# Kernel tuning notes

Hardware: AMD Instinct MI355X
Metric: run time of the kernel (lower is better)

Reference implementation:

```python
import jax, jax.numpy as jnp
import numpy as np

NUM_EXPERTS = 8
TOP_K = 2
RMS_EPS = 1e-6
SCALING = NUM_EXPERTS / TOP_K


def setup_inputs() -> dict:
    key = jax.random.key(0)
    ks = jax.random.split(key, 6)
    B, S, H, I, E = 4, 2048, 2048, 1024, NUM_EXPERTS
    return {
        "hidden_states": jax.random.normal(ks[0], (B, S, H), dtype=jnp.float32),
        "norm_w": jnp.ones((H,), dtype=jnp.float32),
        "router_w": jax.random.normal(ks[1], (E, H), dtype=jnp.float32) * 0.02,
        "gate_w": jax.random.normal(ks[2], (E, I, H), dtype=jnp.float32) * 0.02,
        "up_w": jax.random.normal(ks[3], (E, I, H), dtype=jnp.float32) * 0.02,
        "down_w": jax.random.normal(ks[4], (E, H, I), dtype=jnp.float32) * 0.02,
    }


def reference(hidden_states, norm_w, router_w, gate_w, up_w, down_w):
    B, S, H = hidden_states.shape
    T = B * S
    flat = hidden_states.reshape(T, H)

    # RMSNorm on router input (fp32 math, as in torch module)
    x32 = flat.astype(jnp.float32)
    var = jnp.mean(x32 * x32, axis=-1, keepdims=True)
    router_input = norm_w * (x32 * jax.lax.rsqrt(var + RMS_EPS))

    # Router: softmax -> top-k -> renormalize
    logits = router_input @ router_w.T                     # [T, E]
    probs = jax.nn.softmax(logits, axis=-1)
    topw, topi = jax.lax.top_k(probs, TOP_K)               # [T, K]
    topw = topw / jnp.sum(topw, axis=-1, keepdims=True)

    # Expert combine: per-token weight for expert e (0 if not selected).
    # Running every token through every expert with weight-0 masking is
    # mathematically identical to the gather/scatter dispatch.
    out = jnp.zeros_like(flat)
    for e in range(NUM_EXPERTS):
        w_e = jnp.sum(jnp.where(topi == e, topw, 0.0), axis=-1)   # [T]
        g = flat @ gate_w[e].T                                    # [T, I]
        u = flat @ up_w[e].T                                      # [T, I]
        o = (jax.nn.silu(g) * u) @ down_w[e].T                    # [T, H]
        out = out + o * w_e[:, None]

    student_output = out.reshape(B, S, H) * SCALING

    # Aux load-balancing loss (training path)
    importance = jnp.sum(probs, axis=0) / T                       # [E]
    load = jnp.sum(topi[..., None] == jnp.arange(NUM_EXPERTS), axis=(0, 1)) / (T * TOP_K)
    aux_loss = jnp.sum(importance * load.astype(jnp.float32)) * NUM_EXPERTS

    return student_output, aux_loss
```

## Files before the change

### kernel.cpp

```cpp
#include <hip/hip_runtime.h>
#include <hip/hip_bf16.h>
#include <cstdint>

#define T_TOKENS 8192
#define H_DIM 2048
#define I_DIM 1024
#define N_EXPERTS 8
#define PAIRS (T_TOKENS * 2)
#define TOT_TILES 144
#define TOT_ROWS (TOT_TILES * 128)

using f32x4 = __attribute__((ext_vector_type(4))) float;
using bfv   = __attribute__((ext_vector_type(8))) short;
using u16x8 = __attribute__((ext_vector_type(8))) unsigned short;

typedef __attribute__((address_space(3))) unsigned int lds_u32;
typedef __attribute__((address_space(1))) unsigned int glb_u32;

__device__ __forceinline__ void gll16(const void* g, void* l) {
  __builtin_amdgcn_global_load_lds((const glb_u32*)g, (lds_u32*)l, 16, 0, 0);
}
#define SB0() __builtin_amdgcn_sched_barrier(0)
#define BAR() __builtin_amdgcn_s_barrier()

__device__ inline unsigned short f2bf(float f) {
  unsigned int u = __float_as_uint(f);
  u += 0x7FFFu + ((u >> 16) & 1u);
  return (unsigned short)(u >> 16);
}

__global__ __launch_bounds__(256) void moe_convert_kernel(
    const float* __restrict__ src, unsigned short* __restrict__ dst, int n8) {
  int i = blockIdx.x * 256 + threadIdx.x;
  if (i >= n8) return;
  size_t o = (size_t)i * 8;
  f32x4 a = *reinterpret_cast<const f32x4*>(src + o);
  f32x4 b = *reinterpret_cast<const f32x4*>(src + o + 4);
  u16x8 r = {f2bf(a[0]), f2bf(a[1]), f2bf(a[2]), f2bf(a[3]),
             f2bf(b[0]), f2bf(b[1]), f2bf(b[2]), f2bf(b[3])};
  *reinterpret_cast<u16x8*>(dst + o) = r;
}

__global__ __launch_bounds__(256) void moe_router_kernel(
    const float* __restrict__ X, const float* __restrict__ norm_w,
    const float* __restrict__ rw, float* __restrict__ probs,
    float* __restrict__ topw, int* __restrict__ topi,
    unsigned int* __restrict__ counts, unsigned short* __restrict__ Xb) {
  int t = blockIdx.x;
  int tid = threadIdx.x;
  const float* x = X + (size_t)t * H_DIM;
  int base = tid * 8;
  f32x4 v0 = *reinterpret_cast<const f32x4*>(x + base);
  f32x4 v1 = *reinterpret_cast<const f32x4*>(x + base + 4);
  u16x8 bx = {f2bf(v0[0]), f2bf(v0[1]), f2bf(v0[2]), f2bf(v0[3]),
              f2bf(v1[0]), f2bf(v1[1]), f2bf(v1[2]), f2bf(v1[3])};
  *reinterpret_cast<u16x8*>(Xb + (size_t)t * H_DIM + base) = bx;
  f32x4 nw0 = *reinterpret_cast<const f32x4*>(norm_w + base);
  f32x4 nw1 = *reinterpret_cast<const f32x4*>(norm_w + base + 4);
  float vals[9];
  vals[0] = v0[0]*v0[0] + v0[1]*v0[1] + v0[2]*v0[2] + v0[3]*v0[3]
          + v1[0]*v1[0] + v1[1]*v1[1] + v1[2]*v1[2] + v1[3]*v1[3];
  f32x4 a0 = v0 * nw0, a1 = v1 * nw1;
#pragma unroll
  for (int e = 0; e < 8; ++e) {
    const float* r = rw + e * H_DIM + base;
    f32x4 r0 = *reinterpret_cast<const f32x4*>(r);
    f32x4 r1 = *reinterpret_cast<const f32x4*>(r + 4);
    f32x4 d = a0 * r0 + a1 * r1;
    vals[e + 1] = d[0] + d[1] + d[2] + d[3];
  }
#pragma unroll
  for (int v = 0; v < 9; ++v) {
    float s = vals[v];
#pragma unroll
    for (int off = 32; off > 0; off >>= 1) s += __shfl_xor(s, off);
    vals[v] = s;
  }
  __shared__ float red[4][9];
  int lane = tid & 63, w = tid >> 6;
  if (lane == 0) {
#pragma unroll
    for (int v = 0; v < 9; ++v) red[w][v] = vals[v];
  }
  __syncthreads();
  if (tid == 0) {
    float tot[9];
#pragma unroll
    for (int v = 0; v < 9; ++v) tot[v] = red[0][v] + red[1][v] + red[2][v] + red[3][v];
    float rs = rsqrtf(tot[0] / (float)H_DIM + 1e-6f);
    float lg[8], mx = -1e30f;
#pragma unroll
    for (int e = 0; e < 8; ++e) { lg[e] = tot[e + 1] * rs; mx = fmaxf(mx, lg[e]); }
    float pe[8], sum = 0.f;
#pragma unroll
    for (int e = 0; e < 8; ++e) { pe[e] = expf(lg[e] - mx); sum += pe[e]; }
    float inv = 1.f / sum;
#pragma unroll
    for (int e = 0; e < 8; ++e) { pe[e] *= inv; probs[t * 8 + e] = pe[e]; }
    int b1 = 0; float p1 = pe[0];
#pragma unroll
    for (int e = 1; e < 8; ++e) if (pe[e] > p1) { p1 = pe[e]; b1 = e; }
    int b2 = -1; float p2 = -1.f;
#pragma unroll
    for (int e = 0; e < 8; ++e) if (e != b1 && pe[e] > p2) { p2 = pe[e]; b2 = e; }
    float wsum = p1 + p2;
    topw[t * 2] = p1 / wsum;
    topw[t * 2 + 1] = p2 / wsum;
    topi[t * 2] = b1;
    topi[t * 2 + 1] = b2;
    atomicAdd(&counts[b1], 1u);
    atomicAdd(&counts[8 + b2], 1u);
  }
}

__global__ __launch_bounds__(256) void moe_importance_kernel(
    const float* __restrict__ probs, float* __restrict__ impSum) {
  int e = blockIdx.x, tid = threadIdx.x;
  float s = 0.f;
  for (int t = tid; t < T_TOKENS; t += 256) s += probs[t * 8 + e];
  __shared__ float red[256];
  red[tid] = s;
  __syncthreads();
  for (int st = 128; st > 0; st >>= 1) {
    if (tid < st) red[tid] += red[tid + st];
    __syncthreads();
  }
  if (tid == 0) impSum[e] = red[0];
}

__global__ void moe_offsets_aux_kernel(const unsigned int* __restrict__ counts,
                                       const float* __restrict__ impSum,
                                       int* __restrict__ tileOff,
                                       float* __restrict__ out_aux) {
  if (threadIdx.x == 0 && blockIdx.x == 0) {
    int acc = 0;
    for (int b = 0; b < 16; ++b) {
      tileOff[b] = acc;
      acc += (int)((counts[b] + 127u) >> 7);
    }
    tileOff[16] = acc;
    float a = 0.f;
    for (int e = 0; e < 8; ++e) {
      float load = (float)(counts[e] + counts[8 + e]) / (float)PAIRS;
      a += (impSum[e] / (float)T_TOKENS) * load;
    }
    out_aux[0] = a * (float)N_EXPERTS;
  }
}

__global__ __launch_bounds__(256) void moe_assign_kernel(
    const int* __restrict__ topi, const int* __restrict__ tileOff,
    unsigned int* __restrict__ cursors, int* __restrict__ row2pair) {
  int p = blockIdx.x * 256 + threadIdx.x;
  if (p >= PAIRS) return;
  int b = topi[p] + 8 * (p & 1);
  unsigned int pos = atomicAdd(&cursors[b], 1u);
  row2pair[tileOff[b] * 128 + (int)pos] = p;
}


__global__ __launch_bounds__(256, 2) void moe_stage_a(
    const unsigned short* __restrict__ Xb,
    const unsigned short* __restrict__ Wg, const unsigned short* __restrict__ Wu,
    const int* __restrict__ row2pair, const int* __restrict__ tileOff,
    unsigned int* __restrict__ workCtr, unsigned short* __restrict__ P) {
  __shared__ __align__(16) unsigned short sAB[2][16384];
  __shared__ int sTok[128];
  __shared__ int sWork;
  const int tid = threadIdx.x;
  const int lane = tid & 63, w = tid >> 6;
  const int lrow = lane & 15, grp = lane >> 4;
  const int sub = lane >> 3;
  const int kcs = ((lane & 7) ^ sub) << 3;
  const int cx = (lane & 7) << 3;
  const int nTiles = tileOff[16];
  const int nWork = nTiles * 16;

  for (;;) {
    if (tid == 0) sWork = (int)atomicAdd(workCtr, 1u);
    __syncthreads();
    const int item = sWork;
    if (item >= nWork) break;
    const int mt = item % nTiles;
    const int nt = item / nTiles;
    int b = 0;
#pragma unroll
    for (int k = 1; k < 16; ++k) if (tileOff[k] <= mt) b = k;
    const int e = b & 7;
    const int row0 = mt * 128;
    if (tid < 128) {
      int pr = row2pair[row0 + tid];
      sTok[tid] = (pr >= 0) ? (pr >> 1) : 0;
    }
    __syncthreads();

    const size_t wbase = (size_t)e * ((size_t)I_DIM * H_DIM);
    const unsigned short* src[8];
#pragma unroll
    for (int i = 0; i < 4; ++i) {
      int row = i * 32 + 8 * w + sub;
      src[i] = Xb + (size_t)sTok[row] * H_DIM + kcs;
    }
#pragma unroll
    for (int i = 4; i < 8; ++i) {
      int brow = (i - 4) * 32 + 8 * w + sub;
      int wq = brow >> 5, r5 = brow & 31;
      int ic = nt * 64 + wq * 16 + (r5 & 15);
      const unsigned short* bp = (r5 & 16) ? Wu : Wg;
      src[i] = bp + wbase + (size_t)ic * H_DIM + kcs;
    }

    f32x4 acc[8][2] = {};

#pragma unroll
    for (int i = 0; i < 8; ++i)
      gll16(src[i], (void*)&sAB[0][(i * 256 + tid) * 8]);

    int cur = 0;
#pragma unroll 1
    for (int kk = 0; kk < 32; ++kk) {
      if (kk < 31) {
#pragma unroll
        for (int i = 0; i < 8; ++i)
          gll16(src[i] + ((kk + 1) << 6), (void*)&sAB[cur ^ 1][(i * 256 + tid) * 8]);
        SB0();
        asm volatile("s_waitcnt vmcnt(8)" ::: "memory");
      } else {
        asm volatile("s_waitcnt vmcnt(0)" ::: "memory");
      }
      SB0();
      BAR();
      SB0();
#pragma unroll
      for (int ks = 0; ks < 2; ++ks) {
        const int co = ((ks * 4 + grp) << 3) ^ cx;
        bfv af[8], bf[2];
#pragma unroll
        for (int m = 0; m < 8; ++m)
          af[m] = *reinterpret_cast<const bfv*>(&sAB[cur][(m * 16 + lrow) * 64 + co]);
#pragma unroll
        for (int n = 0; n < 2; ++n)
          bf[n] = *reinterpret_cast<const bfv*>(
              &sAB[cur][8192 + (w * 32 + n * 16 + lrow) * 64 + co]);
        __builtin_amdgcn_s_setprio(1);
#pragma unroll
        for (int m = 0; m < 8; ++m)
#pragma unroll
          for (int n = 0; n < 2; ++n)
            acc[m][n] = __builtin_amdgcn_mfma_f32_16x16x32_bf16(af[m], bf[n], acc[m][n], 0, 0, 0);
        __builtin_amdgcn_s_setprio(0);
      }
      SB0();
      BAR();
      cur ^= 1;
    }

#pragma unroll
    for (int m = 0; m < 8; ++m) {
#pragma unroll
      for (int j = 0; j < 4; ++j) {
        float g = acc[m][0][j];
        float uu = acc[m][1][j];
        float pv = (g / (1.f + expf(-g))) * uu;
        int row = row0 + m * 16 + grp * 4 + j;
        int col = nt * 64 + w * 16 + lrow;
        P[(size_t)row * I_DIM + col] = f2bf(pv);
      }
    }
  }
}

__global__ __launch_bounds__(256, 2) void moe_stage_b(
    const unsigned short* __restrict__ Pb, const unsigned short* __restrict__ Wd,
    const int* __restrict__ row2pair, const int* __restrict__ tileOff,
    const float* __restrict__ topw, unsigned int* __restrict__ workCtr,
    float* __restrict__ out, int phase) {
  __shared__ __align__(16) unsigned short sAB[2][16384];
  __shared__ int sPair[128];
  __shared__ int sWork;
  const int tid = threadIdx.x;
  const int lane = tid & 63, w = tid >> 6;
  const int lrow = lane & 15, grp = lane >> 4;
  const int sub = lane >> 3;
  const int kcs = ((lane & 7) ^ sub) << 3;
  const int cx = (lane & 7) << 3;
  const int t0 = phase ? tileOff[8] : 0;
  const int t1 = phase ? tileOff[16] : tileOff[8];
  const int nTiles = t1 - t0;
  const int nWork = nTiles * 16;

  for (;;) {
    if (tid == 0) sWork = (int)atomicAdd(workCtr, 1u);
    __syncthreads();
    const int item = sWork;
    if (item >= nWork) break;
    const int mt = t0 + item % nTiles;
    const int nt = item / nTiles;
    int b = 0;
#pragma unroll
    for (int k = 1; k < 16; ++k) if (tileOff[k] <= mt) b = k;
    const int e = b & 7;
    const int row0 = mt * 128, h0 = nt * 128;
    if (tid < 128) sPair[tid] = row2pair[row0 + tid];
    __syncthreads();

    const unsigned short* src[8];
#pragma unroll
    for (int i = 0; i < 4; ++i) {
      int row = i * 32 + 8 * w + sub;
      src[i] = Pb + (size_t)(row0 + row) * I_DIM + kcs;
    }
#pragma unroll
    for (int i = 4; i < 8; ++i) {
      int brow = (i - 4) * 32 + 8 * w + sub;
      src[i] = Wd + (size_t)e * ((size_t)H_DIM * I_DIM) + (size_t)(h0 + brow) * I_DIM + kcs;
    }

    f32x4 acc[8][2] = {};

#pragma unroll
    for (int i = 0; i < 8; ++i)
      gll16(src[i], (void*)&sAB[0][(i * 256 + tid) * 8]);

    int cur = 0;
#pragma unroll 1
    for (int kk = 0; kk < 16; ++kk) {
      if (kk < 15) {
#pragma unroll
        for (int i = 0; i < 8; ++i)
          gll16(src[i] + ((kk + 1) << 6), (void*)&sAB[cur ^ 1][(i * 256 + tid) * 8]);
        SB0();
        asm volatile("s_waitcnt vmcnt(8)" ::: "memory");
      } else {
        asm volatile("s_waitcnt vmcnt(0)" ::: "memory");
      }
      SB0();
      BAR();
      SB0();
#pragma unroll
      for (int ks = 0; ks < 2; ++ks) {
        const int co = ((ks * 4 + grp) << 3) ^ cx;
        bfv af[8], bf[2];
#pragma unroll
        for (int m = 0; m < 8; ++m)
          af[m] = *reinterpret_cast<const bfv*>(&sAB[cur][(m * 16 + lrow) * 64 + co]);
#pragma unroll
        for (int n = 0; n < 2; ++n)
          bf[n] = *reinterpret_cast<const bfv*>(
              &sAB[cur][8192 + (w * 32 + n * 16 + lrow) * 64 + co]);
        __builtin_amdgcn_s_setprio(1);
#pragma unroll
        for (int m = 0; m < 8; ++m)
#pragma unroll
          for (int n = 0; n < 2; ++n)
            acc[m][n] = __builtin_amdgcn_mfma_f32_16x16x32_bf16(af[m], bf[n], acc[m][n], 0, 0, 0);
        __builtin_amdgcn_s_setprio(0);
      }
      SB0();
      BAR();
      cur ^= 1;
    }

#pragma unroll
    for (int m = 0; m < 8; ++m) {
#pragma unroll
      for (int j = 0; j < 4; ++j) {
        int rl = m * 16 + grp * 4 + j;
        int pr = sPair[rl];
        if (pr < 0) continue;
        float wgt = topw[pr] * 4.f;
        float* orow = out + (size_t)(pr >> 1) * H_DIM + h0 + w * 32 + lrow;
        if (phase) {
#pragma unroll
          for (int n = 0; n < 2; ++n) orow[n * 16] += wgt * acc[m][n][j];
        } else {
#pragma unroll
          for (int n = 0; n < 2; ++n) orow[n * 16] = wgt * acc[m][n][j];
        }
      }
    }
  }
}

extern "C" void kernel_launch(void* const* d_in, const int* in_sizes, int n_in,
                              void* d_out, int out_size, void* d_ws, size_t ws_size,
                              hipStream_t stream) {
  const float* X = (const float*)d_in[0];
  const float* norm_w = (const float*)d_in[1];
  const float* router_w = (const float*)d_in[2];
  const float* gate_w = (const float*)d_in[3];
  const float* up_w = (const float*)d_in[4];
  const float* down_w = (const float*)d_in[5];
  float* out = (float*)d_out;

  char* ws = (char*)d_ws;
  unsigned short* P = (unsigned short*)(ws);
  float* probs = (float*)(ws + 37748736);
  float* topw = (float*)(ws + 38010880);
  int* topi = (int*)(ws + 38076416);
  int* row2pair = (int*)(ws + 38141952);
  char* ctrl = ws + 38215680;
  unsigned int* counts = (unsigned int*)(ctrl);
  unsigned int* cursors = (unsigned int*)(ctrl + 64);
  float* impSum = (float*)(ctrl + 128);
  int* tileOff = (int*)(ctrl + 192);
  unsigned int* wcA = (unsigned int*)(ctrl + 384);
  unsigned int* wcB0 = (unsigned int*)(ctrl + 388);
  unsigned int* wcB1 = (unsigned int*)(ctrl + 392);
  unsigned short* W1 = (unsigned short*)(ws + 38216192);
  unsigned short* W2 = (unsigned short*)(ws + 71770624);
  unsigned short* Xb = (unsigned short*)(ws + 105325056);

  hipMemsetAsync(ctrl, 0, 512, stream);
  hipMemsetAsync(row2pair, 0xFF, (size_t)TOT_ROWS * 4, stream);

  const int N8 = (N_EXPERTS * I_DIM * H_DIM) / 8;
  moe_convert_kernel<<<N8 / 256, 256, 0, stream>>>(gate_w, W1, N8);
  moe_convert_kernel<<<N8 / 256, 256, 0, stream>>>(up_w, W2, N8);

  moe_router_kernel<<<T_TOKENS, 256, 0, stream>>>(X, norm_w, router_w, probs, topw, topi,
                                                  counts, Xb);
  moe_importance_kernel<<<N_EXPERTS, 256, 0, stream>>>(probs, impSum);
  moe_offsets_aux_kernel<<<1, 64, 0, stream>>>(counts, impSum, tileOff, out + 16777216);
  moe_assign_kernel<<<PAIRS / 256, 256, 0, stream>>>(topi, tileOff, cursors, row2pair);

  moe_stage_a<<<512, 256, 0, stream>>>(Xb, W1, W2, row2pair, tileOff, wcA, P);
  moe_convert_kernel<<<N8 / 256, 256, 0, stream>>>(down_w, W1, N8);
  moe_stage_b<<<512, 256, 0, stream>>>(P, W1, row2pair, tileOff, topw, wcB0, out, 0);
  moe_stage_b<<<512, 256, 0, stream>>>(P, W1, row2pair, tileOff, topw, wcB1, out, 1);
}
```

Measured before the change: 715.7 us.

## Fuse weight conversion into router, 2x2 warp tiling, single stage-b with combine

Folds the fp32-to-bf16 conversion of gate, up and down weights into the router kernel, removing the separate convert launches. Down weights go to a new workspace region when it is large enough. Both GEMM stages switch from a per-wave 8x2 MFMA tile layout to a 2x2 wave arrangement with 4x4 fragments, cutting redundant LDS A-fragment reads. The two-phase stage_b, with its read-modify-write on the output, becomes one pass that writes per-pair bf16 results, followed by a combine kernel that applies the routing weights. This adds a bf16 round trip on the expert outputs, which costs some precision and extra memory traffic.

Measured after the change: 626.4 us. 1.14x faster.

```diff
diff --git a/kernel.cpp b/kernel.cpp
--- a/kernel.cpp
+++ b/kernel.cpp
@@ -27,6 +27,9 @@
   unsigned int u = __float_as_uint(f);
   u += 0x7FFFu + ((u >> 16) & 1u);
   return (unsigned short)(u >> 16);
+}
+__device__ inline float bf2f(unsigned short u) {
+  return __uint_as_float((unsigned int)u << 16);
 }
 
 __global__ __launch_bounds__(256) void moe_convert_kernel(
@@ -45,9 +48,33 @@
     const float* __restrict__ X, const float* __restrict__ norm_w,
     const float* __restrict__ rw, float* __restrict__ probs,
     float* __restrict__ topw, int* __restrict__ topi,
-    unsigned int* __restrict__ counts, unsigned short* __restrict__ Xb) {
+    unsigned int* __restrict__ counts, unsigned short* __restrict__ Xb,
+    const float* __restrict__ gate_w, const float* __restrict__ up_w,
+    const float* __restrict__ down_w,
+    unsigned short* __restrict__ W1, unsigned short* __restrict__ W2,
+    unsigned short* __restrict__ W3) {
   int t = blockIdx.x;
   int tid = threadIdx.x;
+  {
+    size_t co = (size_t)t * 2048 + tid * 8;
+    f32x4 a = *reinterpret_cast<const f32x4*>(gate_w + co);
+    f32x4 b = *reinterpret_cast<const f32x4*>(gate_w + co + 4);
+    u16x8 r = {f2bf(a[0]), f2bf(a[1]), f2bf(a[2]), f2bf(a[3]),
+               f2bf(b[0]), f2bf(b[1]), f2bf(b[2]), f2bf(b[3])};
+    *reinterpret_cast<u16x8*>(W1 + co) = r;
+    a = *reinterpret_cast<const f32x4*>(up_w + co);
+    b = *reinterpret_cast<const f32x4*>(up_w + co + 4);
+    u16x8 r2 = {f2bf(a[0]), f2bf(a[1]), f2bf(a[2]), f2bf(a[3]),
+                f2bf(b[0]), f2bf(b[1]), f2bf(b[2]), f2bf(b[3])};
+    *reinterpret_cast<u16x8*>(W2 + co) = r2;
+    if (W3) {
+      a = *reinterpret_cast<const f32x4*>(down_w + co);
+      b = *reinterpret_cast<const f32x4*>(down_w + co + 4);
+      u16x8 r3 = {f2bf(a[0]), f2bf(a[1]), f2bf(a[2]), f2bf(a[3]),
+                  f2bf(b[0]), f2bf(b[1]), f2bf(b[2]), f2bf(b[3])};
+      *reinterpret_cast<u16x8*>(W3 + co) = r3;
+    }
+  }
   const float* x = X + (size_t)t * H_DIM;
   int base = tid * 8;
   f32x4 v0 = *reinterpret_cast<const f32x4*>(x + base);
@@ -169,6 +196,7 @@
   __shared__ int sWork;
   const int tid = threadIdx.x;
   const int lane = tid & 63, w = tid >> 6;
+  const int wm = w >> 1, wn = w & 1;
   const int lrow = lane & 15, grp = lane >> 4;
   const int sub = lane >> 3;
   const int kcs = ((lane & 7) ^ sub) << 3;
@@ -204,13 +232,13 @@
 #pragma unroll
     for (int i = 4; i < 8; ++i) {
       int brow = (i - 4) * 32 + 8 * w + sub;
-      int wq = brow >> 5, r5 = brow & 31;
-      int ic = nt * 64 + wq * 16 + (r5 & 15);
-      const unsigned short* bp = (r5 & 16) ? Wu : Wg;
+      int wq = brow >> 6, r6 = brow & 63;
+      int ic = nt * 64 + wq * 32 + (r6 & 31);
+      const unsigned short* bp = (r6 & 32) ? Wu : Wg;
       src[i] = bp + wbase + (size_t)ic * H_DIM + kcs;
     }
 
-    f32x4 acc[8][2] = {};
+    f32x4 acc[4][4] = {};
 
 #pragma unroll
     for (int i = 0; i < 8; ++i)
@@ -234,19 +262,20 @@
 #pragma unroll
       for (int ks = 0; ks < 2; ++ks) {
         const int co = ((ks * 4 + grp) << 3) ^ cx;
-        bfv af[8], bf[2];
-#pragma unroll
-        for (int m = 0; m < 8; ++m)
-          af[m] = *reinterpret_cast<const bfv*>(&sAB[cur][(m * 16 + lrow) * 64 + co]);
-#pragma unroll
-        for (int n = 0; n < 2; ++n)
+        bfv af[4], bf[4];
+#pragma unroll
+        for (int m = 0; m < 4; ++m)
+          af[m] = *reinterpret_cast<const bfv*>(
+              &sAB[cur][(wm * 64 + m * 16 + lrow) * 64 + co]);
+#pragma unroll
+        for (int n = 0; n < 4; ++n)
           bf[n] = *reinterpret_cast<const bfv*>(
-              &sAB[cur][8192 + (w * 32 + n * 16 + lrow) * 64 + co]);
+              &sAB[cur][8192 + (wn * 64 + n * 16 + lrow) * 64 + co]);
         __builtin_amdgcn_s_setprio(1);
 #pragma unroll
-        for (int m = 0; m < 8; ++m)
-#pragma unroll
-          for (int n = 0; n < 2; ++n)
+        for (int m = 0; m < 4; ++m)
+#pragma unroll
+          for (int n = 0; n < 4; ++n)
             acc[m][n] = __builtin_amdgcn_mfma_f32_16x16x32_bf16(af[m], bf[n], acc[m][n], 0, 0, 0);
         __builtin_amdgcn_s_setprio(0);
       }
@@ -256,15 +285,18 @@
     }
 
 #pragma unroll
-    for (int m = 0; m < 8; ++m) {
-#pragma unroll
-      for (int j = 0; j < 4; ++j) {
-        float g = acc[m][0][j];
-        float uu = acc[m][1][j];
-        float pv = (g / (1.f + expf(-g))) * uu;
-        int row = row0 + m * 16 + grp * 4 + j;
-        int col = nt * 64 + w * 16 + lrow;
-        P[(size_t)row * I_DIM + col] = f2bf(pv);
+    for (int m = 0; m < 4; ++m) {
+#pragma unroll
+      for (int n = 0; n < 2; ++n) {
+#pragma unroll
+        for (int j = 0; j < 4; ++j) {
+          float g = acc[m][n][j];
+          float uu = acc[m][n + 2][j];
+          float pv = (g / (1.f + expf(-g))) * uu;
+          int row = row0 + wm * 64 + m * 16 + grp * 4 + j;
+          int col = nt * 64 + wn * 32 + n * 16 + lrow;
+          P[(size_t)row * I_DIM + col] = f2bf(pv);
+        }
       }
     }
   }
@@ -273,20 +305,18 @@
 __global__ __launch_bounds__(256, 2) void moe_stage_b(
     const unsigned short* __restrict__ Pb, const unsigned short* __restrict__ Wd,
     const int* __restrict__ row2pair, const int* __restrict__ tileOff,
-    const float* __restrict__ topw, unsigned int* __restrict__ workCtr,
-    float* __restrict__ out, int phase) {
+    unsigned int* __restrict__ workCtr, unsigned short* __restrict__ Opairs) {
   __shared__ __align__(16) unsigned short sAB[2][16384];
   __shared__ int sPair[128];
   __shared__ int sWork;
   const int tid = threadIdx.x;
   const int lane = tid & 63, w = tid >> 6;
+  const int wm = w >> 1, wn = w & 1;
   const int lrow = lane & 15, grp = lane >> 4;
   const int sub = lane >> 3;
   const int kcs = ((lane & 7) ^ sub) << 3;
   const int cx = (lane & 7) << 3;
-  const int t0 = phase ? tileOff[8] : 0;
-  const int t1 = phase ? tileOff[16] : tileOff[8];
-  const int nTiles = t1 - t0;
+  const int nTiles = tileOff[16];
   const int nWork = nTiles * 16;
 
   for (;;) {
@@ -294,7 +324,7 @@
     __syncthreads();
     const int item = sWork;
     if (item >= nWork) break;
-    const int mt = t0 + item % nTiles;
+    const int mt = item % nTiles;
     const int nt = item / nTiles;
     int b = 0;
 #pragma unroll
@@ -316,7 +346,7 @@
       src[i] = Wd + (size_t)e * ((size_t)H_DIM * I_DIM) + (size_t)(h0 + brow) * I_DIM + kcs;
     }
 
-    f32x4 acc[8][2] = {};
+    f32x4 acc[4][4] = {};
 
 #pragma unroll
     for (int i = 0; i < 8; ++i)
@@ -340,19 +370,20 @@
 #pragma unroll
       for (int ks = 0; ks < 2; ++ks) {
         const int co = ((ks * 4 + grp) << 3) ^ cx;
-        bfv af[8], bf[2];
-#pragma unroll
-        for (int m = 0; m < 8; ++m)
-          af[m] = *reinterpret_cast<const bfv*>(&sAB[cur][(m * 16 + lrow) * 64 + co]);
-#pragma unroll
-        for (int n = 0; n < 2; ++n)
+        bfv af[4], bf[4];
+#pragma unroll
+        for (int m = 0; m < 4; ++m)
+          af[m] = *reinterpret_cast<const bfv*>(
+              &sAB[cur][(wm * 64 + m * 16 + lrow) * 64 + co]);
+#pragma unroll
+        for (int n = 0; n < 4; ++n)
           bf[n] = *reinterpret_cast<const bfv*>(
-              &sAB[cur][8192 + (w * 32 + n * 16 + lrow) * 64 + co]);
+              &sAB[cur][8192 + (wn * 64 + n * 16 + lrow) * 64 + co]);
         __builtin_amdgcn_s_setprio(1);
 #pragma unroll
-        for (int m = 0; m < 8; ++m)
-#pragma unroll
-          for (int n = 0; n < 2; ++n)
+        for (int m = 0; m < 4; ++m)
+#pragma unroll
+          for (int n = 0; n < 4; ++n)
             acc[m][n] = __builtin_amdgcn_mfma_f32_16x16x32_bf16(af[m], bf[n], acc[m][n], 0, 0, 0);
         __builtin_amdgcn_s_setprio(0);
       }
@@ -362,24 +393,38 @@
     }
 
 #pragma unroll
-    for (int m = 0; m < 8; ++m) {
+    for (int m = 0; m < 4; ++m) {
 #pragma unroll
       for (int j = 0; j < 4; ++j) {
-        int rl = m * 16 + grp * 4 + j;
+        int rl = wm * 64 + m * 16 + grp * 4 + j;
         int pr = sPair[rl];
         if (pr < 0) continue;
-        float wgt = topw[pr] * 4.f;
-        float* orow = out + (size_t)(pr >> 1) * H_DIM + h0 + w * 32 + lrow;
-        if (phase) {
-#pragma unroll
-          for (int n = 0; n < 2; ++n) orow[n * 16] += wgt * acc[m][n][j];
-        } else {
-#pragma unroll
-          for (int n = 0; n < 2; ++n) orow[n * 16] = wgt * acc[m][n][j];
-        }
-      }
-    }
-  }
+        unsigned short* orow = Opairs + (size_t)pr * H_DIM + h0 + wn * 64 + lrow;
+#pragma unroll
+        for (int n = 0; n < 4; ++n) orow[n * 16] = f2bf(acc[m][n][j]);
+      }
+    }
+  }
+}
+
+__global__ __launch_bounds__(256) void moe_combine_kernel(
+    const unsigned short* __restrict__ Opairs, const float* __restrict__ topw,
+    float* __restrict__ out) {
+  size_t g = (size_t)blockIdx.x * 256 + threadIdx.x;
+  size_t base = g * 8;
+  int t = (int)(base >> 11);
+  int h = (int)(base & 2047);
+  float w0 = topw[t * 2] * 4.f;
+  float w1 = topw[t * 2 + 1] * 4.f;
+  u16x8 o0 = *reinterpret_cast<const u16x8*>(Opairs + (size_t)(t * 2) * H_DIM + h);
+  u16x8 o1 = *reinterpret_cast<const u16x8*>(Opairs + (size_t)(t * 2 + 1) * H_DIM + h);
+  f32x4 r0, r1;
+#pragma unroll
+  for (int j = 0; j < 4; ++j) r0[j] = w0 * bf2f(o0[j]) + w1 * bf2f(o1[j]);
+#pragma unroll
+  for (int j = 0; j < 4; ++j) r1[j] = w0 * bf2f(o0[4 + j]) + w1 * bf2f(o1[4 + j]);
+  *reinterpret_cast<f32x4*>(out + base) = r0;
+  *reinterpret_cast<f32x4*>(out + base + 4) = r1;
 }
 
 extern "C" void kernel_launch(void* const* d_in, const int* in_sizes, int n_in,
@@ -405,27 +450,32 @@
   float* impSum = (float*)(ctrl + 128);
   int* tileOff = (int*)(ctrl + 192);
   unsigned int* wcA = (unsigned int*)(ctrl + 384);
-  unsigned int* wcB0 = (unsigned int*)(ctrl + 388);
-  unsigned int* wcB1 = (unsigned int*)(ctrl + 392);
+  unsigned int* wcB = (unsigned int*)(ctrl + 388);
   unsigned short* W1 = (unsigned short*)(ws + 38216192);
   unsigned short* W2 = (unsigned short*)(ws + 71770624);
   unsigned short* Xb = (unsigned short*)(ws + 105325056);
+  unsigned short* Opairs = (unsigned short*)(ws + 71770624);
+  unsigned short* W3 = (unsigned short*)(ws + 138879488);
+  const bool w3ok = ws_size >= 172433920ull;
 
   hipMemsetAsync(ctrl, 0, 512, stream);
   hipMemsetAsync(row2pair, 0xFF, (size_t)TOT_ROWS * 4, stream);
 
-  const int N8 = (N_EXPERTS * I_DIM * H_DIM) / 8;
-  moe_convert_kernel<<<N8 / 256, 256, 0, stream>>>(gate_w, W1, N8);
-  moe_convert_kernel<<<N8 / 256, 256, 0, stream>>>(up_w, W2, N8);
-
-  moe_router_kernel<<<T_TOKENS, 256, 0, stream>>>(X, norm_w, router_w, probs, topw, topi,
-                                                  counts, Xb);
+  moe_router_kernel<<<T_TOKENS, 256, 0, stream>>>(
+      X, norm_w, router_w, probs, topw, topi, counts, Xb,
+      gate_w, up_w, down_w, W1, W2, w3ok ? W3 : nullptr);
   moe_importance_kernel<<<N_EXPERTS, 256, 0, stream>>>(probs, impSum);
   moe_offsets_aux_kernel<<<1, 64, 0, stream>>>(counts, impSum, tileOff, out + 16777216);
   moe_assign_kernel<<<PAIRS / 256, 256, 0, stream>>>(topi, tileOff, cursors, row2pair);
 
   moe_stage_a<<<512, 256, 0, stream>>>(Xb, W1, W2, row2pair, tileOff, wcA, P);
-  moe_convert_kernel<<<N8 / 256, 256, 0, stream>>>(down_w, W1, N8);
-  moe_stage_b<<<512, 256, 0, stream>>>(P, W1, row2pair, tileOff, topw, wcB0, out, 0);
-  moe_stage_b<<<512, 256, 0, stream>>>(P, W1, row2pair, tileOff, topw, wcB1, out, 1);
-}
+
+  const unsigned short* DW = W3;
+  if (!w3ok) {
+    const int N8 = (N_EXPERTS * I_DIM * H_DIM) / 8;
+    moe_convert_kernel<<<N8 / 256, 256, 0, stream>>>(down_w, W1, N8);
+    DW = W1;
+  }
+  moe_stage_b<<<512, 256, 0, stream>>>(P, DW, row2pair, tileOff, wcB, Opairs);
+  moe_combine_kernel<<<T_TOKENS, 256, 0, stream>>>(Opairs, topw, out);
+}
```
